# Performance work log

Measured on AMD Instinct MI355X. Metric: run time of the kernel, lower is better.

## Reference

```python
import jax, jax.numpy as jnp
import numpy as np

NB_FEATURES = 256
DIM_HEADS = 64
CHUNK = 128  # chunk length for the causal prefix-sum scan (exact, chunking-invariant)
KERNEL_EPS = 1e-6


def _gaussian_orthogonal(nb_rows, nb_cols, seed=0):
    # Mirrors gaussian_orthogonal_random_matrix with scaling=0.
    rng = np.random.default_rng(seed)
    blocks = []
    n_full = nb_rows // nb_cols
    for _ in range(n_full):
        q, _ = np.linalg.qr(rng.standard_normal((nb_cols, nb_cols)))
        blocks.append(q.T)
    rem = nb_rows - n_full * nb_cols
    if rem > 0:
        q, _ = np.linalg.qr(rng.standard_normal((nb_cols, nb_cols)))
        blocks.append(q.T[:rem])
    mat = np.concatenate(blocks, 0)
    multiplier = np.linalg.norm(rng.standard_normal((nb_rows, nb_cols)), axis=1)
    return (multiplier[:, None] * mat).astype(np.float32)


def setup_inputs() -> dict:
    key = jax.random.key(0)
    kq, kk, kv = jax.random.split(key, 3)
    shape = (2, 8, 4096, DIM_HEADS)  # [b, h, n, d]
    return {
        "q": jax.random.normal(kq, shape, dtype=jnp.float32),
        "k": jax.random.normal(kk, shape, dtype=jnp.float32),
        "v": jax.random.normal(kv, shape, dtype=jnp.float32),
        "proj": jnp.asarray(_gaussian_orthogonal(NB_FEATURES, DIM_HEADS)),
    }


def _generalized_kernel(x, proj):
    # generalized_kernel with kernel_fn=sigmoid, normalize_data=True
    normalizer = x.shape[-1] ** (-0.25)
    scores = jnp.einsum('bhnd,md->bhnm', normalizer * x, proj)
    return jax.nn.sigmoid(scores) + KERNEL_EPS


def _causal_linear_attention(qp, kp, v):
    # Exact causal linear attention: out_n = q'_n . (sum_{m<=n} k'_m v_m^T) / (q'_n . (cumsum k')_n + eps-term)
    b, h, n, m = qp.shape
    e = v.shape[-1]
    nc = n // CHUNK

    def split(t):
        return jnp.moveaxis(t.reshape(b, h, nc, CHUNK, t.shape[-1]), 2, 0)

    qs, ks, vs = split(qp), split(kp), split(v)

    def step(carry, xs):
        k_last, S_last = carry              # [b,h,m], [b,h,m,e]
        qc, kc, vc = xs                     # [b,h,c,m], [b,h,c,m], [b,h,c,e]
        k_cum = k_last[:, :, None, :] + jnp.cumsum(kc, axis=2)
        D_inv = 1.0 / jnp.einsum('bhcm,bhcm->bhc', qc, k_cum + KERNEL_EPS)
        ctx = jnp.einsum('bhcm,bhce->bhcme', kc, vc)          # per-position outer products
        S_cum = S_last[:, :, None] + jnp.cumsum(ctx, axis=2)  # running state [b,h,c,m,e]
        out = jnp.einsum('bhcme,bhcm,bhc->bhce', S_cum, qc, D_inv)
        return (k_cum[:, :, -1], S_cum[:, :, -1]), out

    init = (jnp.zeros((b, h, m), qp.dtype), jnp.zeros((b, h, m, e), qp.dtype))
    _, outs = jax.lax.scan(step, init, (qs, ks, vs))          # [nc,b,h,c,e]
    return jnp.moveaxis(outs, 0, 2).reshape(b, h, n, e)


def reference(q, k, v, proj):
    qp = _generalized_kernel(q, proj)
    kp = _generalized_kernel(k, proj)
    return _causal_linear_attention(qp, kp, v)
```

## Files before the change

kernel.cpp:

```cpp
#include <hip/hip_runtime.h>
#include <hip/hip_bf16.h>

#define NORM 0.35355339059327373f
#define EPS 1e-6f

typedef __attribute__((ext_vector_type(8))) short short8;
typedef __attribute__((ext_vector_type(4))) float floatx4;

static __device__ __forceinline__ ushort f2bf(float x) {
  union { __hip_bfloat16 h; ushort u; } c;
  c.h = __float2bfloat16(x);
  return c.u;
}
static __device__ __forceinline__ ushort2 f2bf2(float a, float b) {
  union { __hip_bfloat162 h; ushort2 u; } c;
  c.h = __float22bfloat162_rn(make_float2(a, b));
  return c.u;
}
static __device__ __forceinline__ float sigm(float s) {
  return __builtin_amdgcn_rcpf(1.f + __expf(-s)) + EPS;
}
#define MFMA __builtin_amdgcn_mfma_f32_16x16x32_bf16


__global__ __launch_bounds__(256) void k0_proj(const float* __restrict__ proj,
                                               ushort* __restrict__ prjg) {
  int id = blockIdx.x * 256 + threadIdx.x;
  float4 a = ((const float4*)proj)[id];
  ushort2 lo = f2bf2(a.x * NORM, a.y * NORM);
  ushort2 hi = f2bf2(a.z * NORM, a.w * NORM);
  ((ushort4*)prjg)[id] = make_ushort4(lo.x, lo.y, hi.x, hi.y);
}

__global__ __launch_bounds__(1024) void k1_chunksums(
    const float* __restrict__ k, const float* __restrict__ v,
    const ushort* __restrict__ prjg, float* __restrict__ ksumg,
    ushort* __restrict__ stg) {
  __shared__ __align__(16) ushort xk[128 * 72];
  __shared__ __align__(16) ushort prjl[256 * 72];
  __shared__ __align__(16) ushort kpt[256 * 136];
  __shared__ __align__(16) ushort vt[80 * 136];
  const int t = threadIdx.x;
  const int w = t >> 6, wq = w & 7, wh = w >> 3;
  const int l = t & 63, lr = l & 15, lg = l >> 4;
  const int blk = blockIdx.x;
  const float* kg = k + (size_t)blk * 8192;
  const float* vg = v + (size_t)blk * 8192;

  for (int id = t; id < 2048; id += 1024) {
    float4 a = ((const float4*)kg)[id];
    int row = id >> 4, c = (id & 15) * 4;
    ushort2 p0 = f2bf2(a.x, a.y), p1 = f2bf2(a.z, a.w);
    *(ushort4*)&xk[row * 72 + c] = make_ushort4(p0.x, p0.y, p1.x, p1.y);
  }
  for (int id = t; id < 4096; id += 1024) {
    int row = id >> 4, c = (id & 15) * 4;
    *(ushort4*)&prjl[row * 72 + c] = ((const ushort4*)prjg)[id];
  }
  for (int id = t; id < 2048; id += 1024) {
    float4 a = ((const float4*)vg)[id];
    int pos = id >> 4, e = (id & 15) * 4;
    vt[(e + 0) * 136 + pos] = f2bf(a.x);
    vt[(e + 1) * 136 + pos] = f2bf(a.y);
    vt[(e + 2) * 136 + pos] = f2bf(a.z);
    vt[(e + 3) * 136 + pos] = f2bf(a.w);
  }
  for (int id = t; id < 2048; id += 1024) {
    int rr = id >> 7, pos = id & 127;
    vt[(64 + rr) * 136 + pos] = (rr == 0) ? (ushort)0x3F80 : (ushort)0;
  }
  __syncthreads();

  floatx4 acc[8];
  #pragma unroll
  for (int i = 0; i < 8; ++i) acc[i] = (floatx4){0.f, 0.f, 0.f, 0.f};
  #pragma unroll
  for (int ks = 0; ks < 2; ++ks) {
    short8 a = *(const short8*)&xk[(wq * 16 + lr) * 72 + ks * 32 + lg * 8];
    #pragma unroll
    for (int fb8 = 0; fb8 < 8; ++fb8) {
      int fb = wh * 8 + fb8;
      short8 b = *(const short8*)&prjl[(fb * 16 + lr) * 72 + ks * 32 + lg * 8];
      acc[fb8] = MFMA(a, b, acc[fb8], 0, 0, 0);
    }
  }
  #pragma unroll
  for (int fb8 = 0; fb8 < 8; ++fb8) {
    int fb = wh * 8 + fb8;
    ushort2 p0 = f2bf2(sigm(acc[fb8][0]), sigm(acc[fb8][1]));
    ushort2 p1 = f2bf2(sigm(acc[fb8][2]), sigm(acc[fb8][3]));
    *(ushort4*)&kpt[(fb * 16 + lr) * 136 + wq * 16 + lg * 4] =
        make_ushort4(p0.x, p0.y, p1.x, p1.y);
  }
  __syncthreads();

  floatx4 sacc[5];
  #pragma unroll
  for (int i = 0; i < 5; ++i) sacc[i] = (floatx4){0.f, 0.f, 0.f, 0.f};
  #pragma unroll
  for (int ks = 0; ks < 4; ++ks) {
    short8 a = *(const short8*)&kpt[(w * 16 + lr) * 136 + ks * 32 + lg * 8];
    #pragma unroll
    for (int ebb = 0; ebb < 5; ++ebb) {
      short8 b = *(const short8*)&vt[(ebb * 16 + lr) * 136 + ks * 32 + lg * 8];
      sacc[ebb] = MFMA(a, b, sacc[ebb], 0, 0, 0);
    }
  }
  ushort* stb = stg + (size_t)blk * 16384;
  #pragma unroll
  for (int ebb = 0; ebb < 4; ++ebb) {
    ushort2 p0 = f2bf2(sacc[ebb][0], sacc[ebb][1]);
    ushort2 p1 = f2bf2(sacc[ebb][2], sacc[ebb][3]);
    *(ushort4*)&stb[(size_t)(ebb * 16 + lr) * 256 + w * 16 + lg * 4] =
        make_ushort4(p0.x, p0.y, p1.x, p1.y);
  }
  if (lr == 0) {
    float* kb = ksumg + (size_t)blk * 256;
    #pragma unroll
    for (int r = 0; r < 4; ++r) kb[w * 16 + lg * 4 + r] = sacc[4][r];
  }
}

__global__ __launch_bounds__(256) void k2_scan(float* __restrict__ ksumg,
                                               ushort* __restrict__ stg) {
  int bh = blockIdx.x / 33, part = blockIdx.x % 33, t = threadIdx.x;
  if (part < 32) {
    int e2 = part * 256 + t;
    uint* p = (uint*)stg + (size_t)bh * 32 * 8192 + e2;
    float r0 = 0.f, r1 = 0.f;
    #pragma unroll 4
    for (int c = 0; c < 32; ++c) {
      uint u = p[(size_t)c * 8192];
      float a = __uint_as_float(u << 16);
      float b = __uint_as_float(u & 0xffff0000u);
      ushort2 w2 = f2bf2(r0, r1);
      p[(size_t)c * 8192] = (uint)w2.x | ((uint)w2.y << 16);
      r0 += a; r1 += b;
    }
  } else {
    float run = 0.f;
    float* p = ksumg + (size_t)bh * 32 * 256 + t;
    #pragma unroll 4
    for (int c = 0; c < 32; ++c) {
      float tmp = p[(size_t)c * 256];
      p[(size_t)c * 256] = run;
      run += tmp;
    }
  }
}

__global__ __launch_bounds__(1024) void k3_out(
    const float* __restrict__ q, const float* __restrict__ k,
    const float* __restrict__ v, const ushort* __restrict__ prjg,
    const float* __restrict__ ksumg, const ushort* __restrict__ stg,
    float* __restrict__ out) {
  __shared__ __align__(16) union {
    struct { ushort xq[128 * 72]; ushort xk[128 * 72]; ushort prjh[128 * 72]; } p1;
    struct { ushort ab[128 * 136]; ushort vt[64 * 136]; } p2;
  } r0;
  __shared__ __align__(16) ushort qp[128 * 136];
  __shared__ __align__(16) ushort kp[144 * 136];
  __shared__ __align__(16) ushort sth[64 * 136];
  __shared__ float den[128];

  const int t = threadIdx.x;
  const int w = t >> 6, wq = w & 7, wh = w >> 3;
  const int l = t & 63, lr = l & 15, lg = l >> 4;
  const int blk = blockIdx.x;
  const float* qg = q + (size_t)blk * 8192;
  const float* kg = k + (size_t)blk * 8192;
  const float* vg = v + (size_t)blk * 8192;
  const float* ksb = ksumg + (size_t)blk * 256;
  const ushort* stb = stg + (size_t)blk * 16384;
  float* outg = out + (size_t)blk * 8192;

  for (int id = t; id < 2048; id += 1024) {
    float4 a = ((const float4*)qg)[id];
    float4 c = ((const float4*)kg)[id];
    int row = id >> 4, cc = (id & 15) * 4;
    ushort2 q0 = f2bf2(a.x, a.y), q1 = f2bf2(a.z, a.w);
    ushort2 c0 = f2bf2(c.x, c.y), c1 = f2bf2(c.z, c.w);
    *(ushort4*)&r0.p1.xq[row * 72 + cc] = make_ushort4(q0.x, q0.y, q1.x, q1.y);
    *(ushort4*)&r0.p1.xk[row * 72 + cc] = make_ushort4(c0.x, c0.y, c1.x, c1.y);
  }

  floatx4 Aacc[9];
  floatx4 Oacc[4];
  #pragma unroll
  for (int i = 0; i < 9; ++i) Aacc[i] = (floatx4){0.f, 0.f, 0.f, 0.f};
  #pragma unroll
  for (int i = 0; i < 4; ++i) Oacc[i] = (floatx4){0.f, 0.f, 0.f, 0.f};
  const int eb = wq & 3, qj = wq >> 2;

  for (int fh = 0; fh < 2; ++fh) {
    for (int id = t; id < 2048; id += 1024) {
      int row = id >> 4;
      *(ushort4*)&r0.p1.prjh[row * 72 + (id & 15) * 4] =
          ((const ushort4*)prjg)[fh * 2048 + id];
    }
    for (int id = t; id < 2048; id += 1024) {
      int row = id >> 5, c4 = id & 31;
      *(ushort4*)&sth[row * 136 + c4 * 4] =
          ((const ushort4*)stb)[row * 64 + fh * 32 + c4];
    }
    for (int id = t; id < 2048; id += 1024) {
      int rr = id >> 7, f = id & 127;
      kp[(128 + rr) * 136 + f] = (rr == 0) ? f2bf(ksb[fh * 128 + f] + EPS) : (ushort)0;
    }
    __syncthreads();

    {
      const ushort* xb = wh ? r0.p1.xk : r0.p1.xq;
      ushort* xp = wh ? kp : qp;
      floatx4 fa[8];
      #pragma unroll
      for (int i = 0; i < 8; ++i) fa[i] = (floatx4){0.f, 0.f, 0.f, 0.f};
      #pragma unroll
      for (int ks = 0; ks < 2; ++ks) {
        short8 a = *(const short8*)&r0.p1.prjh[(wq * 16 + lr) * 72 + ks * 32 + lg * 8];
        #pragma unroll
        for (int nb = 0; nb < 8; ++nb) {
          short8 b = *(const short8*)&xb[(nb * 16 + lr) * 72 + ks * 32 + lg * 8];
          fa[nb] = MFMA(a, b, fa[nb], 0, 0, 0);
        }
      }
      #pragma unroll
      for (int nb = 0; nb < 8; ++nb) {
        ushort2 p0 = f2bf2(sigm(fa[nb][0]), sigm(fa[nb][1]));
        ushort2 p1 = f2bf2(sigm(fa[nb][2]), sigm(fa[nb][3]));
        *(ushort4*)&xp[(nb * 16 + lr) * 136 + wq * 16 + lg * 4] =
            make_ushort4(p0.x, p0.y, p1.x, p1.y);
      }
    }
    __syncthreads();

    if (wh == 0) {
      #pragma unroll
      for (int ks = 0; ks < 4; ++ks) {
        short8 aq = *(const short8*)&qp[(wq * 16 + lr) * 136 + ks * 32 + lg * 8];
        #pragma unroll
        for (int nb = 0; nb < 8; ++nb) {
          if (nb <= wq) {
            short8 bk = *(const short8*)&kp[(nb * 16 + lr) * 136 + ks * 32 + lg * 8];
            Aacc[nb] = MFMA(aq, bk, Aacc[nb], 0, 0, 0);
          }
        }
        short8 bx = *(const short8*)&kp[(128 + lr) * 136 + ks * 32 + lg * 8];
        Aacc[8] = MFMA(aq, bx, Aacc[8], 0, 0, 0);
      }
    } else {
      #pragma unroll
      for (int ks = 0; ks < 4; ++ks) {
        short8 as = *(const short8*)&sth[(eb * 16 + lr) * 136 + ks * 32 + lg * 8];
        #pragma unroll
        for (int nq = 0; nq < 4; ++nq) {
          int jb = qj * 4 + nq;
          short8 bq = *(const short8*)&qp[(jb * 16 + lr) * 136 + ks * 32 + lg * 8];
          Oacc[nq] = MFMA(as, bq, Oacc[nq], 0, 0, 0);
        }
      }
    }
    __syncthreads();
  }

  if (wh == 0) {
    #pragma unroll
    for (int r = 0; r < 4; ++r) {
      const int qrow = wq * 16 + lg * 4 + r;
      float s = 0.f;
      #pragma unroll
      for (int nb = 0; nb < 8; ++nb) {
        float val = Aacc[nb][r];
        if (nb * 16 + lr > qrow) val = 0.f;
        Aacc[nb][r] = val;
        s += val;
      }
      s += __shfl_xor(s, 1); s += __shfl_xor(s, 2);
      s += __shfl_xor(s, 4); s += __shfl_xor(s, 8);
      if (lr == 0) den[qrow] = s + Aacc[8][r];
    }
    #pragma unroll
    for (int nb = 0; nb < 8; ++nb) {
      #pragma unroll
      for (int r = 0; r < 4; ++r) {
        r0.p2.ab[(wq * 16 + lg * 4 + r) * 136 + nb * 16 + lr] = f2bf(Aacc[nb][r]);
      }
    }
  } else {
    for (int id = t - 512; id < 2048; id += 512) {
      float4 a = ((const float4*)vg)[id];
      int pos = id >> 4, e = (id & 15) * 4;
      r0.p2.vt[(e + 0) * 136 + pos] = f2bf(a.x);
      r0.p2.vt[(e + 1) * 136 + pos] = f2bf(a.y);
      r0.p2.vt[(e + 2) * 136 + pos] = f2bf(a.z);
      r0.p2.vt[(e + 3) * 136 + pos] = f2bf(a.w);
    }
  }
  __syncthreads();

  if (wh == 1) {
    #pragma unroll
    for (int ks = 0; ks < 4; ++ks) {
      short8 av = *(const short8*)&r0.p2.vt[(eb * 16 + lr) * 136 + ks * 32 + lg * 8];
      #pragma unroll
      for (int nq = 0; nq < 4; ++nq) {
        int jb = qj * 4 + nq;
        if (ks <= (jb >> 1)) {
          short8 ba = *(const short8*)&r0.p2.ab[(jb * 16 + lr) * 136 + ks * 32 + lg * 8];
          Oacc[nq] = MFMA(av, ba, Oacc[nq], 0, 0, 0);
        }
      }
    }
    #pragma unroll
    for (int nq = 0; nq < 4; ++nq) {
      const int qrow = (qj * 4 + nq) * 16 + lr;
      float dinv = __builtin_amdgcn_rcpf(den[qrow]);
      float4 o = make_float4(Oacc[nq][0] * dinv, Oacc[nq][1] * dinv,
                             Oacc[nq][2] * dinv, Oacc[nq][3] * dinv);
      *(float4*)(outg + (size_t)qrow * 64 + eb * 16 + lg * 4) = o;
    }
  }
}

extern "C" void kernel_launch(void* const* d_in, const int* in_sizes, int n_in,
                              void* d_out, int out_size, void* d_ws, size_t ws_size,
                              hipStream_t stream) {
  const float* q = (const float*)d_in[0];
  const float* k = (const float*)d_in[1];
  const float* v = (const float*)d_in[2];
  const float* proj = (const float*)d_in[3];
  float* out = (float*)d_out;
  ushort* prjg = (ushort*)d_ws;
  float* ksumg = (float*)((char*)d_ws + 32768);
  ushort* stg = (ushort*)((char*)d_ws + 32768 + 524288);

  k0_proj<<<16, 256, 0, stream>>>(proj, prjg);
  k1_chunksums<<<512, 1024, 0, stream>>>(k, v, prjg, ksumg, stg);
  k2_scan<<<16 * 33, 256, 0, stream>>>(ksumg, stg);
  k3_out<<<512, 1024, 0, stream>>>(q, k, v, prjg, ksumg, stg, out);
}
```

Measured before the change: 78.09 us.

## Prefetch all k3_out global inputs into registers up front and raise waves-per-EU hint

New measurement: 82.66 us. +5.9%, slower.

```diff
diff --git a/kernel.cpp b/kernel.cpp
--- a/kernel.cpp
+++ b/kernel.cpp
@@ -32,7 +32,7 @@
   ((ushort4*)prjg)[id] = make_ushort4(lo.x, lo.y, hi.x, hi.y);
 }
 
-__global__ __launch_bounds__(1024) void k1_chunksums(
+__global__ __launch_bounds__(1024, 4) void k1_chunksums(
     const float* __restrict__ k, const float* __restrict__ v,
     const ushort* __restrict__ prjg, float* __restrict__ ksumg,
     ushort* __restrict__ stg) {
@@ -149,7 +149,7 @@
   }
 }
 
-__global__ __launch_bounds__(1024) void k3_out(
+__global__ __launch_bounds__(1024, 4) void k3_out(
     const float* __restrict__ q, const float* __restrict__ k,
     const float* __restrict__ v, const ushort* __restrict__ prjg,
     const float* __restrict__ ksumg, const ushort* __restrict__ stg,
@@ -167,21 +167,41 @@
   const int w = t >> 6, wq = w & 7, wh = w >> 3;
   const int l = t & 63, lr = l & 15, lg = l >> 4;
   const int blk = blockIdx.x;
-  const float* qg = q + (size_t)blk * 8192;
-  const float* kg = k + (size_t)blk * 8192;
-  const float* vg = v + (size_t)blk * 8192;
+  const float4* qg4 = (const float4*)(q + (size_t)blk * 8192);
+  const float4* kg4 = (const float4*)(k + (size_t)blk * 8192);
+  const float4* vg4 = (const float4*)(v + (size_t)blk * 8192);
   const float* ksb = ksumg + (size_t)blk * 256;
-  const ushort* stb = stg + (size_t)blk * 16384;
+  const ushort4* st4 = (const ushort4*)(stg + (size_t)blk * 16384);
+  const ushort4* pj4 = (const ushort4*)prjg;
   float* outg = out + (size_t)blk * 8192;
 
-  for (int id = t; id < 2048; id += 1024) {
-    float4 a = ((const float4*)qg)[id];
-    float4 c = ((const float4*)kg)[id];
-    int row = id >> 4, cc = (id & 15) * 4;
-    ushort2 q0 = f2bf2(a.x, a.y), q1 = f2bf2(a.z, a.w);
-    ushort2 c0 = f2bf2(c.x, c.y), c1 = f2bf2(c.z, c.w);
-    *(ushort4*)&r0.p1.xq[row * 72 + cc] = make_ushort4(q0.x, q0.y, q1.x, q1.y);
-    *(ushort4*)&r0.p1.xk[row * 72 + cc] = make_ushort4(c0.x, c0.y, c1.x, c1.y);
+  float4 qa = qg4[t], qb = qg4[t + 1024];
+  float4 ka = kg4[t], kb = kg4[t + 1024];
+  ushort4 p0a = pj4[t], p0b = pj4[t + 1024];
+  ushort4 s0a = st4[(t >> 5) * 64 + (t & 31)];
+  ushort4 s0b = st4[((t >> 5) + 32) * 64 + (t & 31)];
+  float ksv0 = (t < 128) ? ksb[t] : 0.f;
+  ushort4 p1a = pj4[2048 + t], p1b = pj4[2048 + t + 1024];
+  ushort4 s1a = st4[(t >> 5) * 64 + 32 + (t & 31)];
+  ushort4 s1b = st4[((t >> 5) + 32) * 64 + 32 + (t & 31)];
+  float ksv1 = (t < 128) ? ksb[128 + t] : 0.f;
+  float4 fv0, fv1, fv2, fv3;
+  if (wh == 1) {
+    int vid = t - 512;
+    fv0 = vg4[vid]; fv1 = vg4[vid + 512];
+    fv2 = vg4[vid + 1024]; fv3 = vg4[vid + 1536];
+  }
+
+  {
+    int row = t >> 4, cc = (t & 15) * 4;
+    ushort2 a0 = f2bf2(qa.x, qa.y), a1 = f2bf2(qa.z, qa.w);
+    *(ushort4*)&r0.p1.xq[row * 72 + cc] = make_ushort4(a0.x, a0.y, a1.x, a1.y);
+    ushort2 b0 = f2bf2(ka.x, ka.y), b1 = f2bf2(ka.z, ka.w);
+    *(ushort4*)&r0.p1.xk[row * 72 + cc] = make_ushort4(b0.x, b0.y, b1.x, b1.y);
+    ushort2 c0 = f2bf2(qb.x, qb.y), c1 = f2bf2(qb.z, qb.w);
+    *(ushort4*)&r0.p1.xq[(row + 64) * 72 + cc] = make_ushort4(c0.x, c0.y, c1.x, c1.y);
+    ushort2 d0 = f2bf2(kb.x, kb.y), d1 = f2bf2(kb.z, kb.w);
+    *(ushort4*)&r0.p1.xk[(row + 64) * 72 + cc] = make_ushort4(d0.x, d0.y, d1.x, d1.y);
   }
 
   floatx4 Aacc[9];
@@ -192,20 +212,19 @@
   for (int i = 0; i < 4; ++i) Oacc[i] = (floatx4){0.f, 0.f, 0.f, 0.f};
   const int eb = wq & 3, qj = wq >> 2;
 
+  #pragma unroll
   for (int fh = 0; fh < 2; ++fh) {
-    for (int id = t; id < 2048; id += 1024) {
-      int row = id >> 4;
-      *(ushort4*)&r0.p1.prjh[row * 72 + (id & 15) * 4] =
-          ((const ushort4*)prjg)[fh * 2048 + id];
-    }
-    for (int id = t; id < 2048; id += 1024) {
-      int row = id >> 5, c4 = id & 31;
-      *(ushort4*)&sth[row * 136 + c4 * 4] =
-          ((const ushort4*)stb)[row * 64 + fh * 32 + c4];
-    }
-    for (int id = t; id < 2048; id += 1024) {
-      int rr = id >> 7, f = id & 127;
-      kp[(128 + rr) * 136 + f] = (rr == 0) ? f2bf(ksb[fh * 128 + f] + EPS) : (ushort)0;
+    {
+      int row = t >> 4, cc = (t & 15) * 4;
+      *(ushort4*)&r0.p1.prjh[row * 72 + cc] = fh ? p1a : p0a;
+      *(ushort4*)&r0.p1.prjh[(row + 64) * 72 + cc] = fh ? p1b : p0b;
+      int srow = t >> 5, sc = (t & 31) * 4;
+      *(ushort4*)&sth[srow * 136 + sc] = fh ? s1a : s0a;
+      *(ushort4*)&sth[(srow + 32) * 136 + sc] = fh ? s1b : s0b;
+      int rr = t >> 7, f = t & 127;
+      kp[(128 + rr) * 136 + f] =
+          (rr == 0) ? f2bf((fh ? ksv1 : ksv0) + EPS) : (ushort)0;
+      kp[(136 + rr) * 136 + f] = (ushort)0;
     }
     __syncthreads();
 
@@ -287,8 +306,11 @@
       }
     }
   } else {
-    for (int id = t - 512; id < 2048; id += 512) {
-      float4 a = ((const float4*)vg)[id];
+    int vid = t - 512;
+    #pragma unroll
+    for (int u = 0; u < 4; ++u) {
+      float4 a = (u == 0) ? fv0 : (u == 1) ? fv1 : (u == 2) ? fv2 : fv3;
+      int id = vid + u * 512;
       int pos = id >> 4, e = (id & 15) * 4;
       r0.p2.vt[(e + 0) * 136 + pos] = f2bf(a.x);
       r0.p2.vt[(e + 1) * 136 + pos] = f2bf(a.y);
```
